# Kernel tuning notes

Measured on AMD Instinct MI355X. Metric: run time of the kernel, lower is better.

Reference implementation:

```python
import jax, jax.numpy as jnp
import numpy as np
import math

N = 50000      # nodes
E = 800000     # edges
IN = 64        # in_channels
HID = 128      # hidden_channels
OUT = 64       # out_channels
RATIO = 0.8
K = int(math.ceil(RATIO * N))  # 40000 nodes kept after TopKPooling


def setup_inputs() -> dict:
    key = jax.random.key(0)
    ks = jax.random.split(key, 12)
    x = jax.random.normal(ks[0], (N, IN), jnp.float32)
    edge_index = jax.random.randint(ks[1], (2, E), 0, N, dtype=jnp.int32)
    batch = jnp.zeros((N,), jnp.int32)  # single graph

    def glorot(k, fi, fo):
        return jax.random.normal(k, (fi, fo), jnp.float32) * (1.0 / np.sqrt(fi))

    W1 = glorot(ks[2], IN, HID);  b1 = jnp.zeros((HID,), jnp.float32)
    pool_w = jax.random.normal(ks[3], (HID,), jnp.float32) * (1.0 / np.sqrt(HID))
    W2 = glorot(ks[4], HID, OUT); b2 = jnp.zeros((OUT,), jnp.float32)
    W3 = glorot(ks[5], OUT, HID); b3 = jnp.zeros((HID,), jnp.float32)
    W4 = glorot(ks[6], HID, IN);  b4 = jnp.zeros((IN,), jnp.float32)
    return dict(x=x, edge_index=edge_index, batch=batch,
                W1=W1, b1=b1, pool_w=pool_w, W2=W2, b2=b2,
                W3=W3, b3=b3, W4=W4, b4=b4)


def gcn_conv(x, src, dst, ew, W, b, n):
    """PyG GCNConv: D^{-1/2}(A+I)D^{-1/2} X W + b; ew is a 0/1 edge mask."""
    h = x @ W                                             # [n, d_out]
    deg = 1.0 + jax.ops.segment_sum(ew, dst, num_segments=n)  # self-loop adds 1
    dis = jax.lax.rsqrt(deg)
    norm = dis[src] * dis[dst] * ew                       # [E]
    agg = jax.ops.segment_sum(norm[:, None] * h[src], dst, num_segments=n)
    agg = agg + h * (dis * dis)[:, None]                  # self-loop: norm = 1/deg
    return agg + b


def reference(x, edge_index, batch, W1, b1, pool_w, W2, b2, W3, b3, W4, b4):
    src, dst = edge_index[0], edge_index[1]
    ew = jnp.ones((E,), x.dtype)

    # conv1 + relu
    h = jax.nn.relu(gcn_conv(x, src, dst, ew, W1, b1, N))

    # TopKPooling(ratio=0.8): score = tanh(x.w/||w||), keep top-K, scale x by score
    score = jnp.tanh(h @ pool_w / jnp.linalg.norm(pool_w))  # [N]
    vals, perm = jax.lax.top_k(score, K)
    hp = h[perm] * vals[:, None]                            # [K, HID]
    # remap edges to pooled node ids; drop edges touching removed nodes via mask
    new_idx = jnp.full((N,), -1, jnp.int32).at[perm].set(jnp.arange(K, dtype=jnp.int32))
    ns, nd = new_idx[src], new_idx[dst]
    valid = ((ns >= 0) & (nd >= 0)).astype(x.dtype)
    ns = jnp.maximum(ns, 0)
    nd = jnp.maximum(nd, 0)

    h2 = jax.nn.relu(gcn_conv(hp, ns, nd, valid, W2, b2, K))
    h3 = jax.nn.relu(gcn_conv(h2, ns, nd, valid, W3, b3, K))
    h4 = gcn_conv(h3, ns, nd, valid, W4, b4, K)             # [K, IN]

    # global_mean_pool over the (single) graph -> [1, IN]
    return jnp.mean(h4, axis=0, keepdims=True)
```

## Files before the change

### kernel.cpp

```cpp
#include <hip/hip_runtime.h>
#include <hip/hip_bf16.h>
#include <stdint.h>

#define N_NODES 50000
#define N_EDGES 800000
#define K_KEEP  40000
#define BKT     196
#define BCAP    6144

typedef unsigned long long u64;
typedef unsigned int u32;
typedef unsigned short u16;
typedef __hip_bfloat16 bf16;
typedef __hip_bfloat162 bf16x2;
typedef __attribute__((ext_vector_type(8))) short short8;
typedef __attribute__((ext_vector_type(8))) unsigned short ushort8;
typedef __attribute__((ext_vector_type(4))) float f32x4;

struct Ctl {
  u64 prefix;
  u32 kremain;
  u32 cnt;
  float inv_norm;
  u32 isfp32;
  u32 done;
  u32 pad;
  u32 gen;
  u32 done2;
  u32 hist[256];
};

__device__ __forceinline__ float bf2f(bf16 v) { return __bfloat162float(v); }
__device__ __forceinline__ float bfbits2f(unsigned short u) {
  return __uint_as_float(((u32)u) << 16);
}
__device__ __forceinline__ float loadF(const void* p, size_t i, bool f32) {
  return f32 ? ((const float*)p)[i] : bf2f(((const bf16*)p)[i]);
}
__device__ __forceinline__ short f2bf_bits(float f) {
  bf16 t = __float2bfloat16(f);
  return *(const short*)&t;
}

__device__ __forceinline__ void gather_row8_pre(const ushort8* __restrict__ H, int d, int lane,
                                                const int* __restrict__ rowstart,
                                                const int* __restrict__ len,
                                                const int* __restrict__ csr,
                                                float* acc)
{
  ushort8 v = H[(size_t)d * 8 + lane];
  #pragma unroll
  for (int c = 0; c < 8; ++c) acc[c] = bfbits2f(v[c]);
  int i = rowstart[d];
  int i1 = len ? (i + len[d]) : rowstart[d + 1];
  for (; i + 4 <= i1; i += 4) {
    int s0 = csr[i], s1 = csr[i + 1], s2 = csr[i + 2], s3 = csr[i + 3];
    ushort8 v0 = H[(size_t)s0 * 8 + lane];
    ushort8 v1 = H[(size_t)s1 * 8 + lane];
    ushort8 v2 = H[(size_t)s2 * 8 + lane];
    ushort8 v3 = H[(size_t)s3 * 8 + lane];
    #pragma unroll
    for (int c = 0; c < 8; ++c) {
      acc[c] += (bfbits2f(v0[c]) + bfbits2f(v1[c]))
              + (bfbits2f(v2[c]) + bfbits2f(v3[c]));
    }
  }
  for (; i < i1; ++i) {
    int s = csr[i];
    ushort8 vv = H[(size_t)s * 8 + lane];
    #pragma unroll
    for (int c = 0; c < 8; ++c) acc[c] += bfbits2f(vv[c]);
  }
}


__global__ void init_kernel(const unsigned short* __restrict__ x16,
                            int* __restrict__ bucket_cur, int* __restrict__ detcnt, Ctl* ctl) {
  __shared__ u32 dsh[256];
  int i = blockIdx.x * 256 + threadIdx.x;
  if (i < BKT) bucket_cur[i] = i * BCAP;
  if (blockIdx.x == 0) {
    ctl->hist[threadIdx.x] = 0u;
    if (threadIdx.x == 0) {
      ctl->prefix = 0ull; ctl->kremain = K_KEEP; ctl->cnt = 0u;
      ctl->done = 0u; ctl->pad = 0u; ctl->gen = 0u; ctl->done2 = 0u;
    }
  }
  if (blockIdx.x < 64) {
    int base = blockIdx.x * 2048;
    u32 c = 0;
    for (int j = threadIdx.x; j < 2048; j += 256) {
      u32 h = x16[base + j];
      if ((h & 0x7F80u) == 0x7F80u) c++;
    }
    dsh[threadIdx.x] = c;
    __syncthreads();
    for (int s = 128; s > 0; s >>= 1) {
      if (threadIdx.x < s) dsh[threadIdx.x] += dsh[threadIdx.x + s];
      __syncthreads();
    }
    if (threadIdx.x == 0) detcnt[blockIdx.x] = (int)dsh[0];
  }
}


__global__ void bucket_scatter_kernel(const int* __restrict__ src, const int* __restrict__ dst,
                                      int* __restrict__ bucket_cur, u32* __restrict__ bucketbuf,
                                      const int* __restrict__ detcnt, const void* __restrict__ pw,
                                      Ctl* ctl)
{
  __shared__ u32 hist[BKT];
  __shared__ u32 base[BKT];
  __shared__ int f32sh;
  __shared__ float ns[128];
  const int tid = threadIdx.x;
  const int e0 = blockIdx.x * 2048;

  if (tid < 64) {
    int dc = detcnt[tid];
    for (int off = 32; off; off >>= 1) dc += __shfl_down(dc, off);
    if (tid == 0) f32sh = (dc >= 16) ? 1 : 0;
  }
  for (int t = tid; t < BKT; t += 256) hist[t] = 0;
  __syncthreads();
  const bool f32in = f32sh != 0;

  #pragma unroll
  for (int j = 0; j < 8; ++j) {
    int e = e0 + j * 256 + tid;
    if (e < N_EDGES) atomicAdd(&hist[dst[e] >> 8], 1u);
  }
  __syncthreads();
  for (int t = tid; t < BKT; t += 256) {
    u32 c = hist[t];
    base[t] = c ? (u32)atomicAdd(&bucket_cur[t], (int)c) : 0u;
    hist[t] = 0;
  }
  __syncthreads();
  #pragma unroll
  for (int j = 0; j < 8; ++j) {
    int e = e0 + j * 256 + tid;
    if (e < N_EDGES) {
      int d = dst[e];
      int b = d >> 8;
      u32 pos = base[b] + atomicAdd(&hist[b], 1u);
      bucketbuf[pos] = ((u32)src[e] << 8) | (u32)(d & 255);
    }
  }
  if (blockIdx.x == 0) {
    if (tid < 128) { float v = loadF(pw, tid, f32in); ns[tid] = v * v; }
    __syncthreads();
    for (int s = 64; s > 0; s >>= 1) {
      if (tid < s) ns[tid] += ns[tid + s];
      __syncthreads();
    }
    if (tid == 0) {
      ctl->inv_norm = 1.0f / sqrtf(ns[0]);
      ctl->isfp32 = f32in ? 1u : 0u;
    }
  }
}


__global__ void csr_from_buckets_kernel(const u32* __restrict__ bucketbuf, const int* __restrict__ bucket_cur,
                                        int* __restrict__ rowstart, float* __restrict__ dis,
                                        int* __restrict__ csr,
                                        const void* __restrict__ x, ushort8* __restrict__ xbf,
                                        const Ctl* __restrict__ ctl)
{
  __shared__ u32 cnt[256];
  __shared__ u32 loc[256];
  __shared__ u32 cur[256];
  __shared__ float disS[256];
  const int b = blockIdx.x;
  const int tid = threadIdx.x;

  int v = (tid < BKT) ? (bucket_cur[tid] - tid * BCAP) : 0;
  loc[tid] = (u32)v;
  __syncthreads();
  for (int off = 1; off < 256; off <<= 1) {
    u32 t = (tid >= off) ? loc[tid - off] : 0;
    __syncthreads();
    loc[tid] += t;
    __syncthreads();
  }
  const int bc = bucket_cur[b] - b * BCAP;
  const int off0 = (int)loc[b] - bc;
  if (b == BKT - 1 && tid == 0) rowstart[N_NODES] = (int)loc[BKT - 1];
  __syncthreads();

  const u32* buf = bucketbuf + (size_t)b * BCAP;
  cnt[tid] = 0;
  __syncthreads();
  for (int i = tid; i < bc; i += 256) atomicAdd(&cnt[buf[i] & 255u], 1u);
  __syncthreads();
  u32 c = cnt[tid];
  loc[tid] = c;
  __syncthreads();
  for (int off = 1; off < 256; off <<= 1) {
    u32 t = (tid >= off) ? loc[tid - off] : 0;
    __syncthreads();
    loc[tid] += t;
    __syncthreads();
  }
  int node = b * 256 + tid;
  u32 excl = loc[tid] - c;
  float ddv = rsqrtf(1.0f + (float)c);
  disS[tid] = ddv;
  if (node < N_NODES) {
    rowstart[node] = off0 + (int)excl;
    dis[node] = ddv;
  }
  cur[tid] = off0 + excl;
  __syncthreads();
  for (int i = tid; i < bc; i += 256) {
    u32 p = buf[i];
    u32 pos = atomicAdd(&cur[p & 255u], 1u);
    csr[pos] = (int)(p >> 8);
  }
  {
    const bool f32in = ctl->isfp32 != 0;
    if (f32in) {
      const float* xf = (const float*)x;
      for (int u = tid; u < 2048; u += 256) {
        int r = u >> 3, lane = u & 7;
        int d = b * 256 + r;
        if (d < N_NODES) {
          float sc = disS[r];
          ushort8 o;
          #pragma unroll
          for (int c2 = 0; c2 < 8; ++c2)
            o[c2] = (u16)f2bf_bits(xf[(size_t)d * 64 + lane * 8 + c2] * sc);
          xbf[(size_t)d * 8 + lane] = o;
        }
      }
    } else {
      const ushort8* xi = (const ushort8*)x;
      for (int u = tid; u < 2048; u += 256) {
        int r = u >> 3, lane = u & 7;
        int d = b * 256 + r;
        if (d < N_NODES) {
          float sc = disS[r];
          ushort8 vv = xi[(size_t)d * 8 + lane];
          ushort8 o;
          #pragma unroll
          for (int c2 = 0; c2 < 8; ++c2)
            o[c2] = (u16)f2bf_bits(bfbits2f(vv[c2]) * sc);
          xbf[(size_t)d * 8 + lane] = o;
        }
      }
    }
  }
}


__global__ void gather_h2_kernel(const bf16* __restrict__ P, const int* __restrict__ rowstart,
                                 const int* __restrict__ len, const int* __restrict__ csr,
                                 const float* __restrict__ dis,
                                 const void* __restrict__ b, const Ctl* __restrict__ ctl,
                                 bf16* __restrict__ P2, int M)
{
  const bool f32 = ctl->isfp32 != 0;
  int gid = blockIdx.x * 256 + threadIdx.x;
  int d = gid >> 3;
  int lane = gid & 7;
  if (d >= M) return;
  const ushort8* H = (const ushort8*)P;
  float acc[8];
  gather_row8_pre(H, d, lane, rowstart, len, csr, acc);
  float dd = dis[d];
  ushort8 outv;
  #pragma unroll
  for (int c = 0; c < 8; ++c) {
    float h = acc[c] * dd + loadF(b, 8 * lane + c, f32);
    outv[c] = (u16)f2bf_bits(fmaxf(h, 0.f) * dd);
  }
  ((ushort8*)P2)[(size_t)d * 8 + lane] = outv;
}


__global__ void gemm_in_kernel(const ushort8* __restrict__ xbf,
                               const int* __restrict__ rowstart, const int* __restrict__ csr,
                               const float* __restrict__ dis,
                               const void* __restrict__ W, const void* __restrict__ b,
                               const void* __restrict__ pw,
                               bf16* __restrict__ Y, const Ctl* __restrict__ ctl,
                               float* __restrict__ score, u64* __restrict__ keys)
{
  __shared__ short Xs[64 * 72];
  __shared__ short Wt[128 * 72];
  __shared__ float bs[128];
  __shared__ float ps[128];
  const bool f32 = ctl->isfp32 != 0;
  const int tid = threadIdx.x;
  const int row0 = blockIdx.x * 64;

  for (int i = tid; i < 64 * 128; i += 256) {
    int k = i >> 7, n = i & 127;
    Wt[n * 72 + k] = f32 ? f2bf_bits(((const float*)W)[i]) : ((const short*)W)[i];
  }
  for (int u = tid; u < 512; u += 256) {
    int r = u >> 3, lane = u & 7;
    int d = row0 + r;
    float acc[8];
    short8 outv;
    if (d < N_NODES) {
      gather_row8_pre(xbf, d, lane, rowstart, nullptr, csr, acc);
      float dd = dis[d];
      #pragma unroll
      for (int c = 0; c < 8; ++c) outv[c] = f2bf_bits(acc[c] * dd);
    } else {
      #pragma unroll
      for (int c = 0; c < 8; ++c) outv[c] = 0;
    }
    *(short8*)&Xs[r * 72 + lane * 8] = outv;
  }
  for (int i = tid; i < 128; i += 256) { bs[i] = loadF(b, i, f32); ps[i] = loadF(pw, i, f32); }
  __syncthreads();

  const int lane = tid & 63;
  const int w = tid >> 6;
  const int l16 = lane & 15;
  const int quad = lane >> 4;
  f32x4 acc[8];
  #pragma unroll
  for (int ct = 0; ct < 8; ++ct) acc[ct] = (f32x4){0.f, 0.f, 0.f, 0.f};
  const int arow = w * 16 + l16;
  #pragma unroll
  for (int kc = 0; kc < 2; ++kc) {
    short8 a = *(short8*)&Xs[arow * 72 + kc * 32 + quad * 8];
    #pragma unroll
    for (int ct = 0; ct < 8; ++ct) {
      short8 bb = *(short8*)&Wt[(ct * 16 + l16) * 72 + kc * 32 + quad * 8];
      acc[ct] = __builtin_amdgcn_mfma_f32_16x16x32_bf16(a, bb, acc[ct], 0, 0, 0);
    }
  }
  float inv_norm = ctl->inv_norm;
  #pragma unroll
  for (int r = 0; r < 4; ++r) {
    int gr = row0 + w * 16 + quad * 4 + r;
    float p = 0.f;
    #pragma unroll
    for (int ct = 0; ct < 8; ++ct) {
      int col = ct * 16 + l16;
      float h = acc[ct][r] + bs[col];
      if (gr < N_NODES) Y[(size_t)gr * 128 + col] = __float2bfloat16(h);
      p += fmaxf(h, 0.f) * ps[col];
    }
    p += __shfl_down(p, 8, 16);
    p += __shfl_down(p, 4, 16);
    p += __shfl_down(p, 2, 16);
    p += __shfl_down(p, 1, 16);
    if (l16 == 0 && gr < N_NODES) {
      float sc = tanhf(p * inv_norm);
      score[gr] = sc;
      u32 u = __float_as_uint(sc);
      u = (u & 0x80000000u) ? ~u : (u | 0x80000000u);
      keys[gr] = (((u64)u) << 16) | (u64)(0xFFFFu - (u32)gr);
    }
  }
}

__global__ void gemm_128_64_kernel(const bf16* __restrict__ X, const void* __restrict__ W,
                                   bf16* __restrict__ Y, const Ctl* __restrict__ ctl,
                                   int M, int relu_x,
                                   const int* __restrict__ kept, const float* __restrict__ score,
                                   const float* __restrict__ prescale)
{
  __shared__ short Xs[64 * 136];
  __shared__ short Wt[64 * 136];
  __shared__ int keptS[64];
  __shared__ float scS[64];
  const bool f32 = ctl->isfp32 != 0;
  const int tid = threadIdx.x;
  const int row0 = blockIdx.x * 64;

  if (kept) {
    for (int i = tid; i < 64; i += 256) {
      int o = kept[row0 + i];
      keptS[i] = o;
      scS[i] = score[o];
    }
  }
  __syncthreads();

  for (int i = tid; i < 128 * 64; i += 256) {
    int k = i >> 6, n = i & 63;
    Wt[n * 136 + k] = f32 ? f2bf_bits(((const float*)W)[i]) : ((const short*)W)[i];
  }
  const u32* X2 = (const u32*)X;
  for (int p = tid; p < 64 * 64; p += 256) {
    int r = p >> 6, kp = p & 63;
    int srow = kept ? keptS[r] : (row0 + r);
    u32 v = X2[(size_t)srow * 64 + kp];
    if (relu_x) {
      if (v & 0x8000u) v &= 0xFFFF0000u;
      if (v & 0x80000000u) v &= 0x0000FFFFu;
    }
    if (kept) {
      bf16x2 h = *(bf16x2*)&v;
      float s = scS[r];
      bf16x2 o;
      o.x = __float2bfloat16(fmaxf(bf2f(h.x), 0.f) * s);
      o.y = __float2bfloat16(fmaxf(bf2f(h.y), 0.f) * s);
      v = *(u32*)&o;
    }
    *(u32*)&Xs[r * 136 + 2 * kp] = v;
  }
  __syncthreads();

  const int lane = tid & 63;
  const int w = tid >> 6;
  const int l16 = lane & 15;
  const int quad = lane >> 4;
  f32x4 acc[4];
  #pragma unroll
  for (int ct = 0; ct < 4; ++ct) acc[ct] = (f32x4){0.f, 0.f, 0.f, 0.f};
  const int arow = w * 16 + l16;
  #pragma unroll
  for (int kc = 0; kc < 4; ++kc) {
    short8 a = *(short8*)&Xs[arow * 136 + kc * 32 + quad * 8];
    #pragma unroll
    for (int ct = 0; ct < 4; ++ct) {
      short8 bb = *(short8*)&Wt[(ct * 16 + l16) * 136 + kc * 32 + quad * 8];
      acc[ct] = __builtin_amdgcn_mfma_f32_16x16x32_bf16(a, bb, acc[ct], 0, 0, 0);
    }
  }
  #pragma unroll
  for (int ct = 0; ct < 4; ++ct)
    #pragma unroll
    for (int r = 0; r < 4; ++r) {
      int gr = row0 + w * 16 + quad * 4 + r;
      float val = acc[ct][r];
      if (prescale) val *= prescale[gr];
      Y[(size_t)gr * 64 + ct * 16 + l16] = __float2bfloat16(val);
    }
}

__global__ void gemm_64_128_kernel(const bf16* __restrict__ P2,
                                   const int* __restrict__ rowstart, const int* __restrict__ len,
                                   const int* __restrict__ csr, const float* __restrict__ dis,
                                   const void* __restrict__ W, const void* __restrict__ b,
                                   bf16* __restrict__ Y, const Ctl* __restrict__ ctl, int M)
{
  __shared__ short Xs[64 * 72];
  __shared__ short Wt[128 * 72];
  __shared__ float bs[128];
  const bool f32 = ctl->isfp32 != 0;
  const int tid = threadIdx.x;
  const int row0 = blockIdx.x * 64;

  for (int i = tid; i < 64 * 128; i += 256) {
    int k = i >> 7, n = i & 127;
    Wt[n * 72 + k] = f32 ? f2bf_bits(((const float*)W)[i]) : ((const short*)W)[i];
  }
  {
    const ushort8* H = (const ushort8*)P2;
    for (int u = tid; u < 512; u += 256) {
      int r = u >> 3, lane = u & 7;
      int d = row0 + r;
      float acc[8];
      gather_row8_pre(H, d, lane, rowstart, len, csr, acc);
      float dd = dis[d];
      short8 outv;
      #pragma unroll
      for (int c = 0; c < 8; ++c) outv[c] = f2bf_bits(acc[c] * dd);
      *(short8*)&Xs[r * 72 + lane * 8] = outv;
    }
  }
  for (int i = tid; i < 128; i += 256) bs[i] = loadF(b, i, f32);
  __syncthreads();

  const int lane = tid & 63;
  const int w = tid >> 6;
  const int l16 = lane & 15;
  const int quad = lane >> 4;
  f32x4 acc[8];
  #pragma unroll
  for (int ct = 0; ct < 8; ++ct) acc[ct] = (f32x4){0.f, 0.f, 0.f, 0.f};
  const int arow = w * 16 + l16;
  #pragma unroll
  for (int kc = 0; kc < 2; ++kc) {
    short8 a = *(short8*)&Xs[arow * 72 + kc * 32 + quad * 8];
    #pragma unroll
    for (int ct = 0; ct < 8; ++ct) {
      short8 bb = *(short8*)&Wt[(ct * 16 + l16) * 72 + kc * 32 + quad * 8];
      acc[ct] = __builtin_amdgcn_mfma_f32_16x16x32_bf16(a, bb, acc[ct], 0, 0, 0);
    }
  }
  #pragma unroll
  for (int ct = 0; ct < 8; ++ct)
    #pragma unroll
    for (int r = 0; r < 4; ++r) {
      int gr = row0 + w * 16 + quad * 4 + r;
      int col = ct * 16 + l16;
      Y[(size_t)gr * 128 + col] = __float2bfloat16(acc[ct][r] + bs[col]);
    }
}

__global__ void agg_gather64_final_kernel(const bf16* __restrict__ P, const int* __restrict__ rowstart,
                                          const int* __restrict__ len, const int* __restrict__ csr,
                                          const float* __restrict__ dis,
                                          float* __restrict__ partial, int M, int nblk)
{
  __shared__ float cs[64];
  const int tid = threadIdx.x;
  if (tid < 64) cs[tid] = 0.f;
  __syncthreads();
  const int lane = tid & 7;
  const ushort8* H = (const ushort8*)P;
  float acc[8];
  #pragma unroll
  for (int c = 0; c < 8; ++c) acc[c] = 0.f;
  for (int d = (blockIdx.x * 256 + tid) >> 3; d < M; d += nblk * 32) {
    float rsum[8];
    gather_row8_pre(H, d, lane, rowstart, len, csr, rsum);
    float dd = dis[d];
    #pragma unroll
    for (int c = 0; c < 8; ++c) acc[c] += rsum[c] * dd;
  }
  #pragma unroll
  for (int c = 0; c < 8; ++c) atomicAdd(&cs[8 * lane + c], acc[c]);
  __syncthreads();
  if (tid < 64) partial[(size_t)tid * nblk + blockIdx.x] = cs[tid];
}

__global__ void reduce_out_kernel(const float* __restrict__ partial, const void* __restrict__ b,
                                  const Ctl* __restrict__ ctl, void* __restrict__ out, int nblk)
{
  __shared__ float sh[256];
  int c = blockIdx.x;
  float s = 0.f;
  for (int j = threadIdx.x; j < nblk; j += 256) s += partial[(size_t)c * nblk + j];
  sh[threadIdx.x] = s;
  __syncthreads();
  for (int st = 128; st > 0; st >>= 1) {
    if (threadIdx.x < st) sh[threadIdx.x] += sh[threadIdx.x + st];
    __syncthreads();
  }
  if (threadIdx.x == 0) {
    const bool f32 = ctl->isfp32 != 0;
    float val = sh[0] / (float)K_KEEP + loadF(b, c, f32);
    if (f32) ((float*)out)[c] = val;
    else     ((bf16*)out)[c] = __float2bfloat16(val);
  }
}


__global__ void histpick_kernel(const u64* __restrict__ keys, Ctl* ctl, int shift, int nblocks) {
  __shared__ u32 lh[256];
  __shared__ u32 sfx[256];
  __shared__ int lastflag;
  __shared__ int selsh;
  const int tid = threadIdx.x;
  if (ctl->gen != 0u) return;
  lh[tid] = 0;
  __syncthreads();
  u64 prefix = ctl->prefix;
  int i = blockIdx.x * 256 + tid;
  if (i < N_NODES) {
    u64 key = keys[i];
    if ((key >> (shift + 8)) == (prefix >> (shift + 8)))
      atomicAdd(&lh[(u32)((key >> shift) & 0xFF)], 1u);
  }
  __syncthreads();
  u32 c = lh[tid];
  if (c) atomicAdd(&ctl->hist[tid], c);
  __syncthreads();
  if (tid == 0) {
    __threadfence();
    u32 old = atomicAdd(&ctl->done, 1u);
    lastflag = (old == (u32)(nblocks - 1));
  }
  __syncthreads();
  if (!lastflag) return;
  u32 cc = atomicExch(&ctl->hist[tid], 0u);
  sfx[tid] = cc;
  __syncthreads();
  for (int off = 1; off < 256; off <<= 1) {
    u32 t = (tid + off < 256) ? sfx[tid + off] : 0u;
    __syncthreads();
    sfx[tid] += t;
    __syncthreads();
  }
  u32 kr = ctl->kremain;
  u32 above = (tid < 255) ? sfx[tid + 1] : 0u;
  if (sfx[tid] >= kr && above < kr) selsh = tid;
  __syncthreads();
  if (tid == 0) {
    int sel = selsh;
    u32 ab = (sel < 255) ? sfx[sel + 1] : 0u;
    u32 newkr = kr - ab;
    u32 bucketcnt = sfx[sel] - ab;
    ctl->kremain = newkr;
    ctl->prefix = prefix | (((u64)(u32)sel) << shift);
    if (newkr == bucketcnt) ctl->gen = 1u;
    ctl->done = 0u;
  }
}

__global__ void mark_kernel(const u64* __restrict__ keys, Ctl* ctl,
                            int* __restrict__ new_idx, int* __restrict__ kept)
{
  int i = blockIdx.x * 256 + threadIdx.x;
  if (i >= N_NODES) return;
  if (keys[i] >= ctl->prefix) {
    int pos = (int)atomicAdd(&ctl->cnt, 1u);
    new_idx[i] = pos;
    kept[pos] = i;
  } else {
    new_idx[i] = -1;
  }
}


__global__ void csr2_build_kernel(const int* __restrict__ kept, const int* __restrict__ rowstart1,
                                  const int* __restrict__ csr1, const int* __restrict__ new_idx,
                                  Ctl* ctl, int* __restrict__ rowstart2, int* __restrict__ len2,
                                  float* __restrict__ dis2, int* __restrict__ csr2)
{
  int kp = blockIdx.x * 256 + threadIdx.x;
  int lane = threadIdx.x & 63;
  int c = 0;
  int i0 = 0, i1 = 0;
  if (kp < K_KEEP) {
    int o = kept[kp];
    i0 = rowstart1[o]; i1 = rowstart1[o + 1];
    int i = i0;
    for (; i + 4 <= i1; i += 4) {
      int s0 = csr1[i], s1 = csr1[i + 1], s2 = csr1[i + 2], s3 = csr1[i + 3];
      c += (new_idx[s0] >= 0) + (new_idx[s1] >= 0) + (new_idx[s2] >= 0) + (new_idx[s3] >= 0);
    }
    for (; i < i1; ++i) c += (new_idx[csr1[i]] >= 0);
  }
  int pre = c;
  #pragma unroll
  for (int off = 1; off < 64; off <<= 1) {
    int t = __shfl_up(pre, off);
    if (lane >= off) pre += t;
  }
  int wtot = __shfl(pre, 63);
  int wbase = 0;
  if (lane == 0) wbase = (int)atomicAdd(&ctl->pad, (u32)wtot);
  wbase = __shfl(wbase, 0);
  int base = wbase + pre - c;
  if (kp < K_KEEP) {
    rowstart2[kp] = base;
    len2[kp] = c;
    dis2[kp] = rsqrtf(1.0f + (float)c);
    int w = base;
    for (int i = i0; i < i1; ++i) {
      int ns = new_idx[csr1[i]];
      if (ns >= 0) csr2[w++] = ns;
    }
  }
}


extern "C" void kernel_launch(void* const* d_in, const int* in_sizes, int n_in,
                              void* d_out, int out_size, void* d_ws, size_t ws_size,
                              hipStream_t stream)
{
  const void* x  = d_in[0];
  const int*  ei = (const int*)d_in[1];
  const void* W1 = d_in[3];
  const void* b1 = d_in[4];
  const void* pw = d_in[5];
  const void* W2 = d_in[6];
  const void* b2 = d_in[7];
  const void* W3 = d_in[8];
  const void* b3 = d_in[9];
  const void* W4 = d_in[10];
  const void* b4 = d_in[11];

  const int* src = ei;
  const int* dst = ei + N_EDGES;

  float* F = (float*)d_ws;
  bf16*  A16       = (bf16*)F;
  bf16*  B16       = (bf16*)(F + 3200000);
  bf16*  C16       = (bf16*)(F + 6400000);
  u32*   xbf       = (u32*)(F + 9000000);
  float* dis1      = F + 10600000;
  float* dis2      = F + 10650000;
  float* score     = F + 10690000;
  u64*   keys      = (u64*)(F + 10740000);
  int*   new_idx   = (int*)(F + 10840000);
  int*   kept      = (int*)(F + 10890000);
  int*   len2      = (int*)(F + 10930000);
  int*   rowstart1 = (int*)(F + 10970000);
  int*   rowstart2 = (int*)(F + 11020004);
  int*   csr1      = (int*)(F + 11060008);
  int*   csr2      = (int*)(F + 11860008);
  Ctl*   ctl       = (Ctl*)(F + 12660008);
  int*   detcnt    = (int*)(F + 12660856);
  int*   bucket_cur= (int*)(F + 12660920);
  u32*   bucketbuf = (u32*)(F + 12726908);
  float* partial   = F + 13931132;

  const int NB1 = (N_NODES + 255) / 256;
  const int EB2 = (N_EDGES + 2047) / 2048;
  const int GB1 = (N_NODES + 63) / 64;
  const int ABK = K_KEEP * 8 / 256;
  const int CB2 = (K_KEEP + 255) / 256;
  const int NBF = 1024;

  init_kernel<<<NB1, 256, 0, stream>>>((const unsigned short*)x, bucket_cur, detcnt, ctl);

  bucket_scatter_kernel<<<EB2, 256, 0, stream>>>(src, dst, bucket_cur, bucketbuf,
                                                 detcnt, pw, ctl);
  csr_from_buckets_kernel<<<BKT, 256, 0, stream>>>(bucketbuf, bucket_cur, rowstart1, dis1, csr1,
                                                   x, (ushort8*)xbf, ctl);

  gemm_in_kernel<<<GB1, 256, 0, stream>>>((const ushort8*)xbf, rowstart1, csr1, dis1,
                                          W1, b1, pw, B16, ctl, score, keys);

  for (int p = 0; p < 6; ++p)
    histpick_kernel<<<NB1, 256, 0, stream>>>(keys, ctl, 40 - 8 * p, NB1);
  mark_kernel<<<NB1, 256, 0, stream>>>(keys, ctl, new_idx, kept);

  csr2_build_kernel<<<CB2, 256, 0, stream>>>(kept, rowstart1, csr1, new_idx, ctl,
                                             rowstart2, len2, dis2, csr2);

  gemm_128_64_kernel<<<K_KEEP / 64, 256, 0, stream>>>(B16, W2, A16, ctl, K_KEEP, 0, kept, score, dis2);
  gather_h2_kernel<<<ABK, 256, 0, stream>>>(A16, rowstart2, len2, csr2, dis2, b2, ctl, C16, K_KEEP);

  gemm_64_128_kernel<<<K_KEEP / 64, 256, 0, stream>>>(C16, rowstart2, len2, csr2, dis2,
                                                      W3, b3, B16, ctl, K_KEEP);

  gemm_128_64_kernel<<<K_KEEP / 64, 256, 0, stream>>>(B16, W4, A16, ctl, K_KEEP, 1, nullptr, nullptr, dis2);
  agg_gather64_final_kernel<<<NBF, 256, 0, stream>>>(A16, rowstart2, len2, csr2, dis2,
                                                     partial, K_KEEP, NBF);
  reduce_out_kernel<<<64, 256, 0, stream>>>(partial, b4, ctl, d_out, NBF);
}
```

Baseline: 319.4 us.

## Fold mark pass into idle histpick launch, widen gather unroll, cache edge loads

Once the top-k radix select has resolved, the next histpick launch performs the node marking itself, and the standalone mark kernel becomes a no-op. This is meant to take the marking work off the serial chain of small launches. The gather loop also gets an 8-way unroll to keep more row loads in flight. The bucket scatter now loads src/dst into registers once instead of reading dst twice. The gen field changes meaning from a flag to a pass index, and the 8-way unroll raises register pressure.

Result: no change. 313.6 us (-1.8%).

```diff
diff --git a/kernel.cpp b/kernel.cpp
--- a/kernel.cpp
+++ b/kernel.cpp
@@ -53,6 +53,25 @@
   for (int c = 0; c < 8; ++c) acc[c] = bfbits2f(v[c]);
   int i = rowstart[d];
   int i1 = len ? (i + len[d]) : rowstart[d + 1];
+  for (; i + 8 <= i1; i += 8) {
+    int s0 = csr[i],     s1 = csr[i + 1], s2 = csr[i + 2], s3 = csr[i + 3];
+    int s4 = csr[i + 4], s5 = csr[i + 5], s6 = csr[i + 6], s7 = csr[i + 7];
+    ushort8 v0 = H[(size_t)s0 * 8 + lane];
+    ushort8 v1 = H[(size_t)s1 * 8 + lane];
+    ushort8 v2 = H[(size_t)s2 * 8 + lane];
+    ushort8 v3 = H[(size_t)s3 * 8 + lane];
+    ushort8 v4 = H[(size_t)s4 * 8 + lane];
+    ushort8 v5 = H[(size_t)s5 * 8 + lane];
+    ushort8 v6 = H[(size_t)s6 * 8 + lane];
+    ushort8 v7 = H[(size_t)s7 * 8 + lane];
+    #pragma unroll
+    for (int c = 0; c < 8; ++c) {
+      acc[c] += (bfbits2f(v0[c]) + bfbits2f(v1[c]))
+              + (bfbits2f(v2[c]) + bfbits2f(v3[c]));
+      acc[c] += (bfbits2f(v4[c]) + bfbits2f(v5[c]))
+              + (bfbits2f(v6[c]) + bfbits2f(v7[c]));
+    }
+  }
   for (; i + 4 <= i1; i += 4) {
     int s0 = csr[i], s1 = csr[i + 1], s2 = csr[i + 2], s3 = csr[i + 3];
     ushort8 v0 = H[(size_t)s0 * 8 + lane];
@@ -125,11 +144,16 @@
   __syncthreads();
   const bool f32in = f32sh != 0;
 
+  int dreg[8], sreg[8];
   #pragma unroll
   for (int j = 0; j < 8; ++j) {
     int e = e0 + j * 256 + tid;
-    if (e < N_EDGES) atomicAdd(&hist[dst[e] >> 8], 1u);
-  }
+    if (e < N_EDGES) { dreg[j] = dst[e]; sreg[j] = src[e]; }
+    else             { dreg[j] = -1;     sreg[j] = 0;      }
+  }
+  #pragma unroll
+  for (int j = 0; j < 8; ++j)
+    if (dreg[j] >= 0) atomicAdd(&hist[dreg[j] >> 8], 1u);
   __syncthreads();
   for (int t = tid; t < BKT; t += 256) {
     u32 c = hist[t];
@@ -139,12 +163,11 @@
   __syncthreads();
   #pragma unroll
   for (int j = 0; j < 8; ++j) {
-    int e = e0 + j * 256 + tid;
-    if (e < N_EDGES) {
-      int d = dst[e];
+    if (dreg[j] >= 0) {
+      int d = dreg[j];
       int b = d >> 8;
       u32 pos = base[b] + atomicAdd(&hist[b], 1u);
-      bucketbuf[pos] = ((u32)src[e] << 8) | (u32)(d & 255);
+      bucketbuf[pos] = ((u32)sreg[j] << 8) | (u32)(d & 255);
     }
   }
   if (blockIdx.x == 0) {
@@ -547,13 +570,33 @@
 }
 
 
-__global__ void histpick_kernel(const u64* __restrict__ keys, Ctl* ctl, int shift, int nblocks) {
+__device__ __forceinline__ void mark_slice(const u64* __restrict__ keys, Ctl* ctl,
+                                           int* __restrict__ new_idx, int* __restrict__ kept,
+                                           int i)
+{
+  if (i >= N_NODES) return;
+  if (keys[i] >= ctl->prefix) {
+    int pos = (int)atomicAdd(&ctl->cnt, 1u);
+    new_idx[i] = pos;
+    kept[pos] = i;
+  } else {
+    new_idx[i] = -1;
+  }
+}
+
+__global__ void histpick_kernel(const u64* __restrict__ keys, Ctl* ctl, int shift, int pass,
+                                int nblocks, int* __restrict__ new_idx, int* __restrict__ kept) {
   __shared__ u32 lh[256];
   __shared__ u32 sfx[256];
   __shared__ int lastflag;
   __shared__ int selsh;
   const int tid = threadIdx.x;
-  if (ctl->gen != 0u) return;
+  const u32 g = ctl->gen;
+  if (g != 0u) {
+    if ((u32)pass == g)
+      mark_slice(keys, ctl, new_idx, kept, blockIdx.x * 256 + tid);
+    return;
+  }
   lh[tid] = 0;
   __syncthreads();
   u64 prefix = ctl->prefix;
@@ -594,7 +637,7 @@
     u32 bucketcnt = sfx[sel] - ab;
     ctl->kremain = newkr;
     ctl->prefix = prefix | (((u64)(u32)sel) << shift);
-    if (newkr == bucketcnt) ctl->gen = 1u;
+    if (newkr == bucketcnt) ctl->gen = (u32)(pass + 1);
     ctl->done = 0u;
   }
 }
@@ -602,15 +645,9 @@
 __global__ void mark_kernel(const u64* __restrict__ keys, Ctl* ctl,
                             int* __restrict__ new_idx, int* __restrict__ kept)
 {
-  int i = blockIdx.x * 256 + threadIdx.x;
-  if (i >= N_NODES) return;
-  if (keys[i] >= ctl->prefix) {
-    int pos = (int)atomicAdd(&ctl->cnt, 1u);
-    new_idx[i] = pos;
-    kept[pos] = i;
-  } else {
-    new_idx[i] = -1;
-  }
+  u32 g = ctl->gen;
+  if (g >= 1u && g <= 5u) return;
+  mark_slice(keys, ctl, new_idx, kept, blockIdx.x * 256 + (int)threadIdx.x);
 }
 
 
@@ -716,7 +753,7 @@
                                           W1, b1, pw, B16, ctl, score, keys);
 
   for (int p = 0; p < 6; ++p)
-    histpick_kernel<<<NB1, 256, 0, stream>>>(keys, ctl, 40 - 8 * p, NB1);
+    histpick_kernel<<<NB1, 256, 0, stream>>>(keys, ctl, 40 - 8 * p, p, NB1, new_idx, kept);
   mark_kernel<<<NB1, 256, 0, stream>>>(keys, ctl, new_idx, kept);
 
   csr2_build_kernel<<<CB2, 256, 0, stream>>>(kept, rowstart1, csr1, new_idx, ctl,
```
